# Kernel tuning notes

Hardware: AMD Instinct MI355X
Metric: run time of the kernel (lower is better)

## Reference

```python
import jax, jax.numpy as jnp
import numpy as np

B, H, S, DH = 2, 16, 2048, 64
MASK_FILL = -10000.0


def setup_inputs() -> dict:
    key = jax.random.key(0)
    kq, kk, kv = jax.random.split(key, 3)
    q = jax.random.normal(kq, (B, H, S, DH), dtype=jnp.float32)
    k = jax.random.normal(kk, (B, H, S, DH), dtype=jnp.float32)
    v = jax.random.normal(kv, (B, H, S, DH), dtype=jnp.float32)
    # causal mask: True where attention is disallowed (upper triangle)
    mask = jnp.triu(jnp.ones((S, S), dtype=jnp.bool_), k=1)
    return {"q": q, "k": k, "v": v, "mask": mask}


def reference(q, k, v, mask):
    scale = 1.0 / jnp.sqrt(jnp.asarray(k.shape[-1], dtype=q.dtype))
    # scores: [B, H, S_q, S_k]
    scores = jnp.einsum("bhqd,bhkd->bhqk", q, k) * scale
    # additive mask: masked_fill on a zeros [S_k, S_v] matrix -> -10000 where mask
    attn_bias = jnp.where(mask, jnp.asarray(MASK_FILL, dtype=k.dtype),
                          jnp.asarray(0.0, dtype=k.dtype))
    scores = scores + attn_bias  # broadcast over batch/heads
    attn = jax.nn.softmax(scores, axis=-1)
    # dropout_rate = 0.0 -> identity
    return jnp.einsum("bhqk,bhkd->bhqd", attn, v)
```

## Files before the change

### kernel.cpp

```cpp
#include <hip/hip_runtime.h>


#define S_LEN  2048
#define DHDIM  64
#define NHEADS 32
#define LDP    72
#define M2     23.083120654223414f
#define QSCALE 0.18033688011117658f

typedef __attribute__((ext_vector_type(8))) short bf16x8;
typedef __attribute__((ext_vector_type(4))) float f32x4;

__device__ __constant__ unsigned char T_QT[48] = {
    31,31,30,15, 30,29,29,28,14, 28,27,27,26,13, 26,25,25,24,12,
    24,23,23,22,11, 22,21,21,20,10, 20,19,19,18,9, 18,17,17,16,8,
    16,7, 6,5,4,3,2,1,0};
__device__ __constant__ unsigned char T_K0[48] = {
    0,16,0,0, 16,0,15,0,0, 15,0,14,0,0, 14,0,13,0,0,
    13,0,12,0,0, 12,0,11,0,0, 11,0,10,0,0, 10,0,9,0,0,
    9,0, 0,0,0,0,0,0,0};
__device__ __constant__ unsigned char T_K1[48] = {
    16,32,16,16, 31,15,30,15,15, 29,14,28,14,14, 27,13,26,13,13,
    25,12,24,12,12, 23,11,22,11,11, 21,10,20,10,10, 19,9,18,9,9,
    17,8, 7,6,5,4,3,2,1};

__device__ __forceinline__ float fast_exp2(float x) {
#if __has_builtin(__builtin_amdgcn_exp2f)
    return __builtin_amdgcn_exp2f(x);
#else
    return exp2f(x);
#endif
}
__device__ __forceinline__ unsigned short f2bf(float f) {
    unsigned u = __float_as_uint(f);
    return (unsigned short)((u + 0x7fffu + ((u >> 16) & 1u)) >> 16);
}
__device__ __forceinline__ void ld8(const float* p, float* f) {
    float4 a = *(const float4*)p, b = *(const float4*)(p + 4);
    f[0]=a.x; f[1]=a.y; f[2]=a.z; f[3]=a.w; f[4]=b.x; f[5]=b.y; f[6]=b.z; f[7]=b.w;
}
__device__ __forceinline__ uint4 pack8(const float* f, float scale) {
    union { uint4 v; unsigned short s[8]; } w;
    #pragma unroll
    for (int j = 0; j < 8; j++) w.s[j] = f2bf(f[j] * scale);
    return w.v;
}
__device__ __forceinline__ unsigned packhi(float a, float b) {
#if __has_builtin(__builtin_amdgcn_perm)
    return __builtin_amdgcn_perm(__float_as_uint(b), __float_as_uint(a), 0x07060302u);
#else
    return (__float_as_uint(a) >> 16) | (__float_as_uint(b) & 0xffff0000u);
#endif
}

__global__ __launch_bounds__(256) void prep(
    const float* __restrict__ Qf, const float* __restrict__ Kf,
    const float* __restrict__ Vf, unsigned short* __restrict__ qb,
    unsigned short* __restrict__ kb, unsigned short* __restrict__ vtb)
{
    const int st = blockIdx.x, bh = blockIdx.y;
    __shared__ unsigned short lt[64][LDP];
    const float* vp = Vf + ((size_t)bh * S_LEN + st * 64) * DHDIM;
    for (int c = threadIdx.x; c < 512; c += 256) {
        int s = c >> 3, d0 = (c & 7) * 8;
        float f[8]; ld8(vp + s * DHDIM + d0, f);
        #pragma unroll
        for (int j = 0; j < 8; j++) {
            int d = d0 + j;
            int col = (s & 7) | ((((s >> 3) ^ (d >> 3)) & 7) << 3);
            lt[d][col] = f2bf(f[j]);
        }
    }
    size_t off = ((size_t)(bh * 32 + st) * 4096) + (size_t)threadIdx.x * 16;
    float f[8];
    ld8(Qf + off, f);     *(uint4*)(qb + off)     = pack8(f, QSCALE);
    ld8(Qf + off + 8, f); *(uint4*)(qb + off + 8) = pack8(f, QSCALE);
    ld8(Kf + off, f);     *(uint4*)(kb + off)     = pack8(f, 1.0f);
    ld8(Kf + off + 8, f); *(uint4*)(kb + off + 8) = pack8(f, 1.0f);
    __syncthreads();
    unsigned short* op = vtb + (size_t)bh * DHDIM * S_LEN + st * 64;
    for (int c = threadIdx.x; c < 512; c += 256) {
        int d = c >> 3, q = c & 7;
        int colc = ((q ^ (d >> 3)) & 7) << 3;
        *(uint4*)(op + (size_t)d * S_LEN + q * 8) = *(const uint4*)&lt[d][colc];
    }
}

__global__ __launch_bounds__(256) void fattn_splitk(
    const unsigned short* __restrict__ Qp, const unsigned short* __restrict__ Kp,
    const unsigned short* __restrict__ Vp,
    float* __restrict__ pO, float* __restrict__ pL, float* __restrict__ O)
{
    __shared__ unsigned short smem[192 * LDP];
    unsigned short (*ks)[LDP]  = (unsigned short(*)[LDP])smem;
    unsigned short (*vts)[LDP] = (unsigned short(*)[LDP])(smem + 64 * LDP);
    unsigned short (*qs)[LDP]  = (unsigned short(*)[LDP])(smem + 128 * LDP);
    unsigned short (*pst)[LDP] = qs;

    const int bh   = blockIdx.x;
    const int rank = blockIdx.y;
    const int qt   = T_QT[rank];
    const int k0   = T_K0[rank];
    const int k1   = T_K1[rank];
    const bool whole = (k1 - k0 == qt + 1);

    const int tid = threadIdx.x;
    const int wave = tid >> 6, lane = tid & 63;
    const int quad = lane >> 4, l16 = lane & 15;

    {
        const unsigned short* src = Qp + ((size_t)bh * S_LEN + qt * 64) * DHDIM;
        for (int c = tid; c < 512; c += 256) {
            int row = c >> 3, c8 = (c & 7) * 8;
            *(uint4*)&qs[row][c8] = *(const uint4*)(src + row * DHDIM + c8);
        }
    }
    __syncthreads();

    const int prow = wave * 16 + l16;
    const bf16x8 bq0 = *(const bf16x8*)&qs[prow][quad * 8];
    const bf16x8 bq1 = *(const bf16x8*)&qs[prow][32 + quad * 8];

    bf16x8 ones;
    #pragma unroll
    for (int j = 0; j < 8; j++) ones[j] = (short)0x3F80;

    f32x4 of[4];
    f32x4 of_l = (f32x4){0.f, 0.f, 0.f, 0.f};
    #pragma unroll
    for (int n = 0; n < 4; n++) of[n] = (f32x4){0.f, 0.f, 0.f, 0.f};

    for (int kt = k0; kt < k1; kt++) {
        __syncthreads();

        const unsigned short* ksrc = Kp + ((size_t)bh * S_LEN + kt * 64) * DHDIM;
        const unsigned short* vsrc = Vp + (size_t)bh * DHDIM * S_LEN + kt * 64;
        for (int c = tid; c < 512; c += 256) {
            int row = c >> 3, c8 = (c & 7) * 8;
            *(uint4*)&ks[row][c8]  = *(const uint4*)(ksrc + row * DHDIM + c8);
            *(uint4*)&vts[row][c8] = *(const uint4*)(vsrc + (size_t)row * S_LEN + c8);
        }
        __syncthreads();

        f32x4 sf[4];
        #pragma unroll
        for (int n = 0; n < 4; n++) {
            bf16x8 ak0 = *(const bf16x8*)&ks[n * 16 + l16][quad * 8];
            bf16x8 ak1 = *(const bf16x8*)&ks[n * 16 + l16][32 + quad * 8];
            sf[n] = (f32x4){-M2, -M2, -M2, -M2};
            sf[n] = __builtin_amdgcn_mfma_f32_16x16x32_bf16(ak0, bq0, sf[n], 0, 0, 0);
            sf[n] = __builtin_amdgcn_mfma_f32_16x16x32_bf16(ak1, bq1, sf[n], 0, 0, 0);
        }

        const bool diag = (kt == qt);
        #pragma unroll
        for (int n = 0; n < 4; n++) {
            float p[4];
            #pragma unroll
            for (int r = 0; r < 4; r++) {
                p[r] = fast_exp2(sf[n][r]);
                if (diag && (n * 16 + quad * 4 + r > prow)) p[r] = 0.f;
            }
            uint2 dw;
            dw.x = packhi(p[0], p[1]);
            dw.y = packhi(p[2], p[3]);
            *(uint2*)&pst[prow][n * 16 + quad * 4] = dw;
        }
        asm volatile("s_waitcnt lgkmcnt(0)" ::: "memory");

        bf16x8 bp0 = *(const bf16x8*)&pst[prow][quad * 8];
        bf16x8 bp1 = *(const bf16x8*)&pst[prow][32 + quad * 8];
        of_l = __builtin_amdgcn_mfma_f32_16x16x32_bf16(ones, bp0, of_l, 0, 0, 0);
        of_l = __builtin_amdgcn_mfma_f32_16x16x32_bf16(ones, bp1, of_l, 0, 0, 0);
        #pragma unroll
        for (int n = 0; n < 4; n++) {
            bf16x8 av0 = *(const bf16x8*)&vts[n * 16 + l16][quad * 8];
            bf16x8 av1 = *(const bf16x8*)&vts[n * 16 + l16][32 + quad * 8];
            of[n] = __builtin_amdgcn_mfma_f32_16x16x32_bf16(av0, bp0, of[n], 0, 0, 0);
            of[n] = __builtin_amdgcn_mfma_f32_16x16x32_bf16(av1, bp1, of[n], 0, 0, 0);
        }
    }

    if (whole) {
        const float inv = 1.f / of_l[0];
        float* op = O + ((size_t)bh * S_LEN + qt * 64 + prow) * DHDIM;
        #pragma unroll
        for (int n = 0; n < 4; n++)
            *(float4*)(op + n * 16 + quad * 4) = make_float4(
                of[n][0] * inv, of[n][1] * inv, of[n][2] * inv, of[n][3] * inv);
    } else {
        const int slot = ((bh * 16 + (qt - 16)) << 1) | (k0 != 0 ? 1 : 0);
        if (quad == 0) pL[slot * 64 + prow] = of_l[0];
        float* op = pO + (size_t)slot * 4096 + prow * 64;
        #pragma unroll
        for (int n = 0; n < 4; n++)
            *(float4*)(op + n * 16 + quad * 4) =
                make_float4(of[n][0], of[n][1], of[n][2], of[n][3]);
    }
}

__global__ __launch_bounds__(256) void combine(
    const float* __restrict__ pO, const float* __restrict__ pL,
    float* __restrict__ O)
{
    const int qt = 16 + blockIdx.x, bh = blockIdx.y;
    const int sa = ((bh * 16 + (qt - 16)) << 1), sb = sa | 1;
    const float* A = pO + (size_t)sa * 4096;
    const float* B = pO + (size_t)sb * 4096;
    float* out = O + ((size_t)bh * S_LEN + qt * 64) * DHDIM;
    #pragma unroll
    for (int k = 0; k < 4; k++) {
        int c = threadIdx.x + k * 256;
        int row = c >> 4;
        float inv = 1.f / (pL[sa * 64 + row] + pL[sb * 64 + row]);
        float4 a = *(const float4*)(A + c * 4);
        float4 b = *(const float4*)(B + c * 4);
        *(float4*)(out + c * 4) = make_float4(
            (a.x + b.x) * inv, (a.y + b.y) * inv,
            (a.z + b.z) * inv, (a.w + b.w) * inv);
    }
}

template <bool PRE>
__global__ __launch_bounds__(256) void fattn_kernel(
    const void* __restrict__ Qp, const void* __restrict__ Kp,
    const void* __restrict__ Vp, float* __restrict__ O)
{
    __shared__ unsigned short smem[192 * LDP];
    unsigned short (*ks)[LDP]  = (unsigned short(*)[LDP])smem;
    unsigned short (*vts)[LDP] = (unsigned short(*)[LDP])(smem + 64 * LDP);
    unsigned short (*qs)[LDP]  = (unsigned short(*)[LDP])(smem + 128 * LDP);
    unsigned short (*pst)[LDP] = qs;

    const int id = blockIdx.y * 32 + blockIdx.x;
    const int g  = id >> 8;
    const int r8 = id & 255;
    const int bh = r8 >> 3;
    const int s8 = r8 & 7;
    const int qt = (g == 0) ? 31 - 2 * s8 : (g == 1) ? 2 * s8
                 : (g == 2) ? 30 - 2 * s8 : 2 * s8 + 1;

    const int tid = threadIdx.x;
    const int wave = tid >> 6, lane = tid & 63;
    const int quad = lane >> 4, l16 = lane & 15;

    if constexpr (PRE) {
        const unsigned short* src = (const unsigned short*)Qp
            + ((size_t)bh * S_LEN + qt * 64) * DHDIM;
        for (int c = tid; c < 512; c += 256) {
            int row = c >> 3, c8 = (c & 7) * 8;
            *(uint4*)&qs[row][c8] = *(const uint4*)(src + row * DHDIM + c8);
        }
    } else {
        const float* src = (const float*)Qp + ((size_t)bh * S_LEN + qt * 64) * DHDIM;
        for (int c = tid; c < 512; c += 256) {
            int row = c >> 3, c8 = (c & 7) * 8;
            float f[8]; ld8(src + row * DHDIM + c8, f);
            *(uint4*)&qs[row][c8] = pack8(f, QSCALE);
        }
    }
    __syncthreads();

    const int prow = wave * 16 + l16;
    const bf16x8 bq0 = *(const bf16x8*)&qs[prow][quad * 8];
    const bf16x8 bq1 = *(const bf16x8*)&qs[prow][32 + quad * 8];

    float l_p = 0.f;
    f32x4 of[4];
    #pragma unroll
    for (int n = 0; n < 4; n++) of[n] = (f32x4){0.f, 0.f, 0.f, 0.f};

    for (int kt = 0; kt <= qt; kt++) {
        __syncthreads();
        if constexpr (PRE) {
            const unsigned short* ksrc = (const unsigned short*)Kp
                + ((size_t)bh * S_LEN + kt * 64) * DHDIM;
            const unsigned short* vsrc = (const unsigned short*)Vp
                + (size_t)bh * DHDIM * S_LEN + kt * 64;
            for (int c = tid; c < 512; c += 256) {
                int row = c >> 3, c8 = (c & 7) * 8;
                *(uint4*)&ks[row][c8]  = *(const uint4*)(ksrc + row * DHDIM + c8);
                *(uint4*)&vts[row][c8] = *(const uint4*)(vsrc + (size_t)row * S_LEN + c8);
            }
        } else {
            const float* ksrc = (const float*)Kp + ((size_t)bh * S_LEN + kt * 64) * DHDIM;
            const float* vsrc = (const float*)Vp + ((size_t)bh * S_LEN + kt * 64) * DHDIM;
            for (int c = tid; c < 512; c += 256) {
                int row = c >> 3, c8 = (c & 7) * 8;
                float f[8];
                ld8(ksrc + row * DHDIM + c8, f);
                *(uint4*)&ks[row][c8] = pack8(f, 1.0f);
                ld8(vsrc + row * DHDIM + c8, f);
                #pragma unroll
                for (int j = 0; j < 8; j++) vts[c8 + j][row] = f2bf(f[j]);
            }
        }
        __syncthreads();

        f32x4 sf[4];
        #pragma unroll
        for (int n = 0; n < 4; n++) {
            bf16x8 ak0 = *(const bf16x8*)&ks[n * 16 + l16][quad * 8];
            bf16x8 ak1 = *(const bf16x8*)&ks[n * 16 + l16][32 + quad * 8];
            sf[n] = (f32x4){-M2, -M2, -M2, -M2};
            sf[n] = __builtin_amdgcn_mfma_f32_16x16x32_bf16(ak0, bq0, sf[n], 0, 0, 0);
            sf[n] = __builtin_amdgcn_mfma_f32_16x16x32_bf16(ak1, bq1, sf[n], 0, 0, 0);
        }

        const bool diag = (kt == qt);
        #pragma unroll
        for (int n = 0; n < 4; n++) {
            float p[4];
            #pragma unroll
            for (int r = 0; r < 4; r++) {
                p[r] = fast_exp2(sf[n][r]);
                if (diag && (n * 16 + quad * 4 + r > prow)) p[r] = 0.f;
                l_p += p[r];
            }
            uint2 dw;
            dw.x = packhi(p[0], p[1]);
            dw.y = packhi(p[2], p[3]);
            *(uint2*)&pst[prow][n * 16 + quad * 4] = dw;
        }
        asm volatile("s_waitcnt lgkmcnt(0)" ::: "memory");

        bf16x8 bp0 = *(const bf16x8*)&pst[prow][quad * 8];
        bf16x8 bp1 = *(const bf16x8*)&pst[prow][32 + quad * 8];
        #pragma unroll
        for (int n = 0; n < 4; n++) {
            bf16x8 av0 = *(const bf16x8*)&vts[n * 16 + l16][quad * 8];
            bf16x8 av1 = *(const bf16x8*)&vts[n * 16 + l16][32 + quad * 8];
            of[n] = __builtin_amdgcn_mfma_f32_16x16x32_bf16(av0, bp0, of[n], 0, 0, 0);
            of[n] = __builtin_amdgcn_mfma_f32_16x16x32_bf16(av1, bp1, of[n], 0, 0, 0);
        }
    }

    l_p += __shfl_xor(l_p, 16);
    l_p += __shfl_xor(l_p, 32);
    const float inv = 1.f / l_p;
    float* op = O + ((size_t)bh * S_LEN + qt * 64 + prow) * DHDIM;
    #pragma unroll
    for (int n = 0; n < 4; n++)
        *(float4*)(op + n * 16 + quad * 4) = make_float4(
            of[n][0] * inv, of[n][1] * inv, of[n][2] * inv, of[n][3] * inv);
}

extern "C" void kernel_launch(void* const* d_in, const int* in_sizes, int n_in,
                              void* d_out, int out_size, void* d_ws, size_t ws_size,
                              hipStream_t stream) {
    const float* Q = (const float*)d_in[0];
    const float* K = (const float*)d_in[1];
    const float* V = (const float*)d_in[2];
    float* O = (float*)d_out;
    const size_t N = (size_t)NHEADS * S_LEN * DHDIM;
    const size_t prepB  = 3 * N * sizeof(unsigned short);
    const size_t partB  = (size_t)1024 * (4096 + 64) * sizeof(float);

    if (d_ws && ws_size >= prepB + partB) {
        unsigned short* qb  = (unsigned short*)d_ws;
        unsigned short* kb  = qb + N;
        unsigned short* vtb = kb + N;
        float* pO = (float*)((char*)d_ws + prepB);
        float* pL = pO + (size_t)1024 * 4096;
        prep<<<dim3(S_LEN / 64, NHEADS), 256, 0, stream>>>(Q, K, V, qb, kb, vtb);
        fattn_splitk<<<dim3(32, 48), 256, 0, stream>>>(qb, kb, vtb, pO, pL, O);
        combine<<<dim3(16, 32), 256, 0, stream>>>(pO, pL, O);
    } else if (d_ws && ws_size >= prepB) {
        unsigned short* qb  = (unsigned short*)d_ws;
        unsigned short* kb  = qb + N;
        unsigned short* vtb = kb + N;
        prep<<<dim3(S_LEN / 64, NHEADS), 256, 0, stream>>>(Q, K, V, qb, kb, vtb);
        fattn_kernel<true><<<dim3(32, 32), 256, 0, stream>>>(qb, kb, vtb, O);
    } else {
        fattn_kernel<false><<<dim3(32, 32), 256, 0, stream>>>(Q, K, V, O);
    }
}
```

Measured before the change: 144.8 us.

## Prefetch next K/V tile into registers and pack V transpose writes

The attention loop now loads the next K and V tile from global memory into registers while the current tile is being computed, then stores it to shared memory at the start of the next iteration. This is meant to hide global load latency behind the MFMA work, at the cost of extra VGPRs per thread. The prep kernel's V transpose now packs two sequence positions into one 32-bit shared memory word, halving the number of shared stores. It also contains an odd no-op ternary in the index.

```diff
diff --git a/kernel.cpp b/kernel.cpp
--- a/kernel.cpp
+++ b/kernel.cpp
@@ -59,16 +59,20 @@
     unsigned short* __restrict__ kb, unsigned short* __restrict__ vtb)
 {
     const int st = blockIdx.x, bh = blockIdx.y;
-    __shared__ unsigned short lt[64][LDP];
+    __shared__ unsigned lt32[64][LDP / 2];
     const float* vp = Vf + ((size_t)bh * S_LEN + st * 64) * DHDIM;
-    for (int c = threadIdx.x; c < 512; c += 256) {
-        int s = c >> 3, d0 = (c & 7) * 8;
-        float f[8]; ld8(vp + s * DHDIM + d0, f);
+    {
+        const int c = threadIdx.x;
+        const int sp = c >> 3;
+        const int d0 = (c & 7) * 8;
+        float fa[8], fb[8];
+        ld8(vp + (2 * sp) * DHDIM + d0, fa);
+        ld8(vp + (2 * sp + 1) * DHDIM + d0, fb);
         #pragma unroll
         for (int j = 0; j < 8; j++) {
             int d = d0 + j;
-            int col = (s & 7) | ((((s >> 3) ^ (d >> 3)) & 7) << 3);
-            lt[d][col] = f2bf(f[j]);
+            int colw = (sp & 3) | ((((sp >> 2) ^ (d >> 3)) & 7) << 2);
+            lt32[d][colw] = (unsigned)f2bf(fa[j]) | ((unsigned)f2bf(fb[j]) << 16);
         }
     }
     size_t off = ((size_t)(bh * 32 + st) * 4096) + (size_t)threadIdx.x * 16;
@@ -81,8 +85,8 @@
     unsigned short* op = vtb + (size_t)bh * DHDIM * S_LEN + st * 64;
     for (int c = threadIdx.x; c < 512; c += 256) {
         int d = c >> 3, q = c & 7;
-        int colc = ((q ^ (d >> 3)) & 7) << 3;
-        *(uint4*)(op + (size_t)d * S_LEN + q * 8) = *(const uint4*)&lt[d][colc];
+        int colw = ((q ^ (d >> 3)) & 7) << 2;
+        *(uint4*)(op + (size_t)d * S_LEN + q * 8) = *(const uint4*)&lt32[d][colw & ~3 ? colw : colw];
     }
 }
 
@@ -130,15 +134,34 @@
     #pragma unroll
     for (int n = 0; n < 4; n++) of[n] = (f32x4){0.f, 0.f, 0.f, 0.f};
 
+    const unsigned short* Kbh = Kp + (size_t)bh * S_LEN * DHDIM;
+    const unsigned short* Vbh = Vp + (size_t)bh * DHDIM * S_LEN;
+    const int sr = tid >> 3, sc = (tid & 7) * 8;
+    uint4 kr0, kr1, vr0, vr1;
+    {
+        const unsigned short* ksrc = Kbh + (size_t)k0 * 64 * DHDIM;
+        const unsigned short* vsrc = Vbh + k0 * 64;
+        kr0 = *(const uint4*)(ksrc + sr * DHDIM + sc);
+        kr1 = *(const uint4*)(ksrc + (sr + 32) * DHDIM + sc);
+        vr0 = *(const uint4*)(vsrc + (size_t)sr * S_LEN + sc);
+        vr1 = *(const uint4*)(vsrc + (size_t)(sr + 32) * S_LEN + sc);
+    }
+
     for (int kt = k0; kt < k1; kt++) {
         __syncthreads();
 
-        const unsigned short* ksrc = Kp + ((size_t)bh * S_LEN + kt * 64) * DHDIM;
-        const unsigned short* vsrc = Vp + (size_t)bh * DHDIM * S_LEN + kt * 64;
-        for (int c = tid; c < 512; c += 256) {
-            int row = c >> 3, c8 = (c & 7) * 8;
-            *(uint4*)&ks[row][c8]  = *(const uint4*)(ksrc + row * DHDIM + c8);
-            *(uint4*)&vts[row][c8] = *(const uint4*)(vsrc + (size_t)row * S_LEN + c8);
+        *(uint4*)&ks[sr][sc]       = kr0;
+        *(uint4*)&ks[sr + 32][sc]  = kr1;
+        *(uint4*)&vts[sr][sc]      = vr0;
+        *(uint4*)&vts[sr + 32][sc] = vr1;
+
+        if (kt + 1 < k1) {
+            const unsigned short* ksrc = Kbh + (size_t)(kt + 1) * 64 * DHDIM;
+            const unsigned short* vsrc = Vbh + (kt + 1) * 64;
+            kr0 = *(const uint4*)(ksrc + sr * DHDIM + sc);
+            kr1 = *(const uint4*)(ksrc + (sr + 32) * DHDIM + sc);
+            vr0 = *(const uint4*)(vsrc + (size_t)sr * S_LEN + sc);
+            vr1 = *(const uint4*)(vsrc + (size_t)(sr + 32) * S_LEN + sc);
         }
         __syncthreads();
 
```

Result: faster. 140.7 us (-2.8%).
